# Kernel tuning notes

Measured on AMD Instinct MI355X. Metric: run time of the kernel, lower is better.

The kernel has to match this reference:

```python
import jax, jax.numpy as jnp
import numpy as np

ALPHA = 0.2        # LeakyReLU slope
N_NODES = 50000
N_REL = 500


def l2norm(x):
    n = jnp.linalg.norm(x, axis=1, keepdims=True)
    return x / jnp.maximum(n, 1e-12)


def gat_layer(x, edge, eemb, a, a2, concat):
    # x: [N, F]; edge: [2, E] (edge[0]=target, edge[1]=source); eemb: [E, R]
    dst = edge[0]
    h = jnp.concatenate([x[dst], x[edge[1]], eemb], axis=1)          # [E, 2F+R]
    m = h @ a.T                                                       # [E, out]
    p = -jax.nn.leaky_relu(m @ a2[0], ALPHA)                          # [E]
    e = jnp.exp(p)
    rowsum = jax.ops.segment_sum(e, dst, num_segments=N_NODES)       # [N]
    rowsum = jnp.where(rowsum == 0.0, 1e-12, rowsum)
    hp = jax.ops.segment_sum(e[:, None] * m, dst, num_segments=N_NODES) / rowsum[:, None]
    return jax.nn.elu(hp) if concat else hp


def setup_inputs() -> dict:
    key = jax.random.key(0)
    ks = jax.random.split(key, 12)
    E, ENH = 150000, 30000
    D, NHID, H = 200, 100, 2
    return {
        "entity_embeddings": jax.random.normal(ks[0], (N_NODES, D), jnp.float32),
        "relation_embeddings": jax.random.normal(ks[1], (N_REL, D), jnp.float32),
        "W_entities": jax.random.normal(ks[2], (D, NHID * H), jnp.float32) * 0.1,
        "W_gat": jax.random.normal(ks[3], (D, NHID * H), jnp.float32) * 0.1,
        "a_heads": jax.random.normal(ks[4], (H, NHID, 2 * D + D), jnp.float32) * 0.1,
        "a2_heads": jax.random.normal(ks[5], (H, 1, NHID), jnp.float32) * 0.1,
        "a_out": jax.random.normal(ks[6], (NHID * H, 3 * NHID * H), jnp.float32) * 0.1,
        "a2_out": jax.random.normal(ks[7], (1, NHID * H), jnp.float32) * 0.1,
        "batch_entities": jax.random.randint(ks[8], (20000,), 0, N_NODES),
        "edge_list": jax.random.randint(ks[9], (2, E), 0, N_NODES),
        "edge_type": jax.random.randint(ks[10], (E,), 0, N_REL),
        "train_indices_nhop": jax.random.randint(ks[11], (ENH, 4), 0, N_REL),
    }


def reference(entity_embeddings, relation_embeddings, W_entities, W_gat,
              a_heads, a2_heads, a_out, a2_out,
              batch_entities, edge_list, edge_type, train_indices_nhop):
    x = l2norm(entity_embeddings)
    # n-hop edges: (target, source) = (col 3, col 0); relation pair = (col 1, col 2)
    edge_nhop = jnp.stack([train_indices_nhop[:, 3], train_indices_nhop[:, 0]])
    edge_all = jnp.concatenate([edge_list, edge_nhop], axis=1)       # [2, E+Enh]
    eemb1 = jnp.concatenate([
        relation_embeddings[edge_type],
        relation_embeddings[train_indices_nhop[:, 1]] + relation_embeddings[train_indices_nhop[:, 2]],
    ], axis=0)
    # multi-head sparse attention (concat=True -> elu inside)
    heads = jax.vmap(lambda a, a2: gat_layer(x, edge_all, eemb1, a, a2, True))(a_heads, a2_heads)
    x1 = jnp.transpose(heads, (1, 0, 2)).reshape(x.shape[0], -1)     # [N, H*nhid]
    out_rel = relation_embeddings @ W_gat                             # [R, H*nhid]
    eemb2 = jnp.concatenate([
        out_rel[edge_type],
        out_rel[train_indices_nhop[:, 1]] + out_rel[train_indices_nhop[:, 2]],
    ], axis=0)
    out_ent = jax.nn.elu(gat_layer(x1, edge_all, eemb2, a_out, a2_out, False))
    mask = jnp.zeros((x.shape[0],), x.dtype).at[batch_entities].set(1.0)
    out_ent = l2norm(x @ W_entities + mask[:, None] * out_ent)
    return out_ent, out_rel, mask
```

## Files before the change

kernel.cpp:

```cpp
#include <hip/hip_runtime.h>
#include <hip/hip_bf16.h>
#include <math.h>

#define DD   200
#define NHID 100
#define OD   200
#define KP   224
#define PBS  224
#define LDSW 40

typedef __attribute__((ext_vector_type(8))) short short8;
typedef __attribute__((ext_vector_type(4))) float f32x4;

static inline int cdiv(int a, int b) { return (a + b - 1) / b; }

__device__ inline float toF(float x) { return x; }
__device__ inline float toF(__hip_bfloat16 x) { return __bfloat162float(x); }
__device__ inline void storeC(float v, float* p) { *p = v; }
__device__ inline void storeC(float v, __hip_bfloat16* p) { *p = __float2bfloat16(v); }
__device__ inline short bf16s(float f) {
    __hip_bfloat16 h = __float2bfloat16(f);
    short s; __builtin_memcpy(&s, &h, 2); return s;
}
__device__ inline float bfLo(unsigned u) { return __uint_as_float(u << 16); }
__device__ inline float bfHi(unsigned u) { return __uint_as_float(u & 0xFFFF0000u); }
__device__ inline float readlaneF(float v, int l) {
    return __uint_as_float((unsigned)__builtin_amdgcn_readlane((int)__float_as_uint(v), l));
}

__global__ __launch_bounds__(256)
void rownorm_inv_k(const float* __restrict__ in, float* __restrict__ sc, int M, int Dd)
{
    int wave = (blockIdx.x * blockDim.x + threadIdx.x) >> 6;
    int lane = threadIdx.x & 63;
    if (wave >= M) return;
    float ss = 0.f;
    for (int k = lane; k < Dd; k += 64) {
        float x = in[(size_t)wave * Dd + k];
        ss += x * x;
    }
    for (int o = 32; o > 0; o >>= 1) ss += __shfl_down(ss, o);
    if (lane == 0) sc[wave] = 1.f / fmaxf(sqrtf(ss), 1e-12f);
}

__global__ void prep_bt_l1(const float* __restrict__ ah, __hip_bfloat16* __restrict__ Bt)
{
    int c = blockIdx.x, k = threadIdx.x;
    if (k >= KP) return;
    int seg = c / 100, idx = c - seg * 100;
    int h = seg & 1, off = (seg >> 1) * 200;
    float v = (k < 200) ? ah[(size_t)(h * 100 + idx) * 600 + off + k] : 0.f;
    Bt[(size_t)c * KP + k] = __float2bfloat16(v);
}
__global__ void prep_bt_l2(const float* __restrict__ ao, __hip_bfloat16* __restrict__ Bt)
{
    int c = blockIdx.x, k = threadIdx.x;
    if (k >= KP) return;
    int row = (c < 200) ? c : c - 200;
    int off = (c < 200) ? 0 : 200;
    float v = (k < 200) ? ao[(size_t)row * 600 + off + k] : 0.f;
    Bt[(size_t)c * KP + k] = __float2bfloat16(v);
}
__global__ void prep_bt_fin(const float* __restrict__ W, __hip_bfloat16* __restrict__ Bt)
{
    int c = blockIdx.x, k = threadIdx.x;
    if (k >= KP) return;
    float v = (c < 200 && k < 200) ? W[(size_t)k * 200 + c] : 0.f;
    Bt[(size_t)c * KP + k] = __float2bfloat16(v);
}

__global__ __launch_bounds__(256)
void l1_both_k(const float* __restrict__ ent, const float* __restrict__ nscale,
               const __hip_bfloat16* __restrict__ Bt,
               const float* __restrict__ a2h,
               __hip_bfloat16* __restrict__ x1,
               __hip_bfloat16* __restrict__ pB,
               float* __restrict__ s1,
               int M)
{
    __shared__ __align__(16) __hip_bfloat16 Bs[400 * LDSW];
    int tid = threadIdx.x, wave = tid >> 6, lane = tid & 63;
    int quad = lane >> 4, l16 = lane & 15;
    int m0 = blockIdx.x * 64;
    int arow = m0 + wave * 16 + l16;
    bool rok = arow < M;
    float nsc = rok ? nscale[arow] : 0.f;
    const float* arp = ent + (size_t)arow * DD;

    f32x4 acc[25];
#pragma unroll
    for (int t = 0; t < 25; t++) acc[t] = (f32x4){0.f, 0.f, 0.f, 0.f};

    short8 stg[7];
#pragma unroll
    for (int i = 0; i < 7; i++) {
        int idx = tid + i * 256;
        if (idx < 1600) {
            int r = idx >> 2, c8 = idx & 3;
            stg[i] = *(const short8*)(Bt + (size_t)r * KP + c8 * 8);
        }
    }

    for (int ch = 0; ch < 7; ch++) {
#pragma unroll
        for (int i = 0; i < 7; i++) {
            int idx = tid + i * 256;
            if (idx < 1600) {
                int r = idx >> 2, c8 = idx & 3;
                *(short8*)(Bs + r * LDSW + c8 * 8) = stg[i];
            }
        }
        __syncthreads();
        if (ch < 6) {
            int kb2 = (ch + 1) * 32;
#pragma unroll
            for (int i = 0; i < 7; i++) {
                int idx = tid + i * 256;
                if (idx < 1600) {
                    int r = idx >> 2, c8 = idx & 3;
                    stg[i] = *(const short8*)(Bt + (size_t)r * KP + kb2 + c8 * 8);
                }
            }
        }
        int kb = ch * 32 + quad * 8;
        float av[8];
        if (rok && kb + 8 <= DD) {
            const float4* p = (const float4*)(arp + kb);
            float4 u0 = p[0], u1 = p[1];
            av[0] = u0.x; av[1] = u0.y; av[2] = u0.z; av[3] = u0.w;
            av[4] = u1.x; av[5] = u1.y; av[6] = u1.z; av[7] = u1.w;
        } else {
#pragma unroll
            for (int j = 0; j < 8; j++) av[j] = (rok && kb + j < DD) ? arp[kb + j] : 0.f;
        }
        short8 a;
#pragma unroll
        for (int j = 0; j < 8; j++) a[j] = bf16s(av[j] * nsc);
        const __hip_bfloat16* bp = Bs + (size_t)l16 * LDSW + quad * 8;
#pragma unroll
        for (int t = 0; t < 25; t++) {
            short8 b = *(const short8*)(bp + (size_t)t * 16 * LDSW);
            acc[t] = __builtin_amdgcn_mfma_f32_16x16x32_bf16(a, b, acc[t], 0, 0, 0);
        }
        __syncthreads();
    }

    int orow = m0 + wave * 16 + quad * 4;
    float d0[4] = {0,0,0,0}, d1[4] = {0,0,0,0}, d2[4] = {0,0,0,0}, d3[4] = {0,0,0,0};
#pragma unroll
    for (int t = 0; t < 25; t++) {
        int c = t * 16 + l16;
        int seg = c / 100, idx = c - seg * 100;
        float w = a2h[(seg & 1) * 100 + idx];
#pragma unroll
        for (int i = 0; i < 4; i++) {
            float v = acc[t][i];
            float vw = v * w;
            if (seg == 0) d0[i] += vw;
            else if (seg == 1) d1[i] += vw;
            else if (seg == 2) d2[i] += vw;
            else d3[i] += vw;
            int gm = orow + i;
            if (gm < M) {
                if (seg < 2) x1[(size_t)gm * KP + c] = __float2bfloat16(v);
                else pB[(size_t)gm * PBS + idx * 2 + (seg - 2)] = __float2bfloat16(v);
            }
        }
    }
#pragma unroll
    for (int msk = 1; msk < 16; msk <<= 1)
#pragma unroll
        for (int i = 0; i < 4; i++) {
            d0[i] += __shfl_xor(d0[i], msk);
            d1[i] += __shfl_xor(d1[i], msk);
            d2[i] += __shfl_xor(d2[i], msk);
            d3[i] += __shfl_xor(d3[i], msk);
        }
    if (l16 == 0)
#pragma unroll
        for (int i = 0; i < 4; i++) {
            int gm = orow + i;
            if (gm < M) {
                s1[gm] = d0[i]; s1[M + gm] = d1[i];
                float2 sv; sv.x = d2[i]; sv.y = d3[i];
                *(float2*)((char*)pB + (size_t)gm * (PBS * 2) + 400) = sv;
            }
        }
}

__global__ __launch_bounds__(256)
void l2_proj_k(const __hip_bfloat16* __restrict__ x1,
               const __hip_bfloat16* __restrict__ Bt,
               const float* __restrict__ a2o,
               float* __restrict__ x1A1,
               __hip_bfloat16* __restrict__ x1A2,
               float* __restrict__ s1, int M)
{
    __shared__ __align__(16) __hip_bfloat16 Bs[400 * LDSW];
    int tid = threadIdx.x, wave = tid >> 6, lane = tid & 63;
    int quad = lane >> 4, l16 = lane & 15;
    int m0 = blockIdx.x * 64;
    int arow = m0 + wave * 16 + l16;
    bool rok = arow < M;
    const __hip_bfloat16* arp = x1 + (size_t)arow * KP;

    f32x4 acc[25];
#pragma unroll
    for (int t = 0; t < 25; t++) acc[t] = (f32x4){0.f, 0.f, 0.f, 0.f};

    short8 stg[7];
#pragma unroll
    for (int i = 0; i < 7; i++) {
        int idx = tid + i * 256;
        if (idx < 1600) {
            int r = idx >> 2, c8 = idx & 3;
            stg[i] = *(const short8*)(Bt + (size_t)r * KP + c8 * 8);
        }
    }

    for (int ch = 0; ch < 7; ch++) {
#pragma unroll
        for (int i = 0; i < 7; i++) {
            int idx = tid + i * 256;
            if (idx < 1600) {
                int r = idx >> 2, c8 = idx & 3;
                *(short8*)(Bs + r * LDSW + c8 * 8) = stg[i];
            }
        }
        __syncthreads();
        if (ch < 6) {
            int kb2 = (ch + 1) * 32;
#pragma unroll
            for (int i = 0; i < 7; i++) {
                int idx = tid + i * 256;
                if (idx < 1600) {
                    int r = idx >> 2, c8 = idx & 3;
                    stg[i] = *(const short8*)(Bt + (size_t)r * KP + kb2 + c8 * 8);
                }
            }
        }
        int kb = ch * 32 + quad * 8;
        short8 a = (short8){0,0,0,0,0,0,0,0};
        if (rok) a = *(const short8*)(arp + kb);
        const __hip_bfloat16* bp = Bs + (size_t)l16 * LDSW + quad * 8;
#pragma unroll
        for (int t = 0; t < 25; t++) {
            short8 b = *(const short8*)(bp + (size_t)t * 16 * LDSW);
            acc[t] = __builtin_amdgcn_mfma_f32_16x16x32_bf16(a, b, acc[t], 0, 0, 0);
        }
        __syncthreads();
    }

    int orow = m0 + wave * 16 + quad * 4;
    float dA[4] = {0,0,0,0}, dB[4] = {0,0,0,0};
#pragma unroll
    for (int t = 0; t < 25; t++) {
        int c = t * 16 + l16;
        bool first = c < 200;
        int cc = first ? c : c - 200;
        float w = a2o[cc];
#pragma unroll
        for (int i = 0; i < 4; i++) {
            float v = acc[t][i];
            int gm = orow + i;
            if (first) {
                dA[i] += v * w;
                if (gm < M) x1A1[(size_t)gm * OD + c] = v;
            } else {
                dB[i] += v * w;
                if (gm < M) x1A2[(size_t)gm * PBS + cc] = __float2bfloat16(v);
            }
        }
    }
#pragma unroll
    for (int msk = 1; msk < 16; msk <<= 1)
#pragma unroll
        for (int i = 0; i < 4; i++) {
            dA[i] += __shfl_xor(dA[i], msk);
            dB[i] += __shfl_xor(dB[i], msk);
        }
    if (l16 == 0)
#pragma unroll
        for (int i = 0; i < 4; i++) {
            int gm = orow + i;
            if (gm < M) {
                s1[gm] = dA[i];
                *(float*)((char*)x1A2 + (size_t)gm * (PBS * 2) + 400) = dB[i];
            }
        }
}

__global__ __launch_bounds__(256)
void final_mfma_k(const float* __restrict__ ent, const float* __restrict__ nscale,
                  const __hip_bfloat16* __restrict__ Bt,
                  float* __restrict__ outent, int M)
{
    __shared__ __align__(16) __hip_bfloat16 Bs[208 * LDSW];
    int tid = threadIdx.x, wave = tid >> 6, lane = tid & 63;
    int quad = lane >> 4, l16 = lane & 15;
    int m0 = blockIdx.x * 64;
    int arow = m0 + wave * 16 + l16;
    bool rok = arow < M;
    float nsc = rok ? nscale[arow] : 0.f;
    const float* arp = ent + (size_t)arow * DD;

    f32x4 acc[13];
#pragma unroll
    for (int t = 0; t < 13; t++) acc[t] = (f32x4){0.f, 0.f, 0.f, 0.f};

    short8 stg[4];
#pragma unroll
    for (int i = 0; i < 4; i++) {
        int idx = tid + i * 256;
        if (idx < 832) {
            int r = idx >> 2, c8 = idx & 3;
            stg[i] = *(const short8*)(Bt + (size_t)r * KP + c8 * 8);
        }
    }

    for (int ch = 0; ch < 7; ch++) {
#pragma unroll
        for (int i = 0; i < 4; i++) {
            int idx = tid + i * 256;
            if (idx < 832) {
                int r = idx >> 2, c8 = idx & 3;
                *(short8*)(Bs + r * LDSW + c8 * 8) = stg[i];
            }
        }
        __syncthreads();
        if (ch < 6) {
            int kb2 = (ch + 1) * 32;
#pragma unroll
            for (int i = 0; i < 4; i++) {
                int idx = tid + i * 256;
                if (idx < 832) {
                    int r = idx >> 2, c8 = idx & 3;
                    stg[i] = *(const short8*)(Bt + (size_t)r * KP + kb2 + c8 * 8);
                }
            }
        }
        int kb = ch * 32 + quad * 8;
        float av[8];
        if (rok && kb + 8 <= DD) {
            const float4* p = (const float4*)(arp + kb);
            float4 u0 = p[0], u1 = p[1];
            av[0] = u0.x; av[1] = u0.y; av[2] = u0.z; av[3] = u0.w;
            av[4] = u1.x; av[5] = u1.y; av[6] = u1.z; av[7] = u1.w;
        } else {
#pragma unroll
            for (int j = 0; j < 8; j++) av[j] = (rok && kb + j < DD) ? arp[kb + j] : 0.f;
        }
        short8 a;
#pragma unroll
        for (int j = 0; j < 8; j++) a[j] = bf16s(av[j] * nsc);
        const __hip_bfloat16* bp = Bs + (size_t)l16 * LDSW + quad * 8;
#pragma unroll
        for (int t = 0; t < 13; t++) {
            short8 b = *(const short8*)(bp + (size_t)t * 16 * LDSW);
            acc[t] = __builtin_amdgcn_mfma_f32_16x16x32_bf16(a, b, acc[t], 0, 0, 0);
        }
        __syncthreads();
    }

    int orow = m0 + wave * 16 + quad * 4;
    float ss[4] = {0.f, 0.f, 0.f, 0.f};
#pragma unroll
    for (int t = 0; t < 13; t++) {
        int gn = t * 16 + l16;
#pragma unroll
        for (int i = 0; i < 4; i++) {
            int gm = orow + i;
            float v = 0.f;
            if (gn < OD && gm < M) v = acc[t][i] + outent[(size_t)gm * OD + gn];
            acc[t][i] = v;
            ss[i] += v * v;
        }
    }
#pragma unroll
    for (int msk = 1; msk < 16; msk <<= 1)
#pragma unroll
        for (int i = 0; i < 4; i++) ss[i] += __shfl_xor(ss[i], msk);
    float scl[4];
#pragma unroll
    for (int i = 0; i < 4; i++) scl[i] = 1.f / fmaxf(sqrtf(ss[i]), 1e-12f);
#pragma unroll
    for (int t = 0; t < 13; t++) {
        int gn = t * 16 + l16;
        if (gn >= OD) continue;
#pragma unroll
        for (int i = 0; i < 4; i++) {
            int gm = orow + i;
            if (gm < M) outent[(size_t)gm * OD + gn] = acc[t][i] * scl[i];
        }
    }
}

#define KPAD 48
template<bool BTr, typename AT, typename CT>
__global__ __launch_bounds__(256)
void gemm_mfma_k(const AT* __restrict__ A, int lda, const float* __restrict__ ascale,
                 const float* __restrict__ B, int ldb, int colOff,
                 CT* __restrict__ C, int ldc, int cs, int co,
                 int M, int Nc, int K)
{
    __shared__ __align__(16) __hip_bfloat16 As[64][KPAD];
    __shared__ __align__(16) __hip_bfloat16 Bs[64][KPAD];
    int tid  = threadIdx.x;
    int wave = tid >> 6, lane = tid & 63;
    int quad = lane >> 4, l16 = lane & 15;
    int n0 = blockIdx.x * 64, m0 = blockIdx.y * 64;
    f32x4 acc[4];
#pragma unroll
    for (int t = 0; t < 4; t++) acc[t] = (f32x4){0.f, 0.f, 0.f, 0.f};

    for (int k0 = 0; k0 < K; k0 += 32) {
        {
            int m = tid >> 2, kc = (tid & 3) * 8;
            int gm = m0 + m;
            float scale = (ascale && gm < M) ? ascale[gm] : 1.f;
#pragma unroll
            for (int j = 0; j < 8; j++) {
                int gk = k0 + kc + j;
                float v = 0.f;
                if (gm < M && gk < K) v = toF(A[(size_t)gm * lda + gk]) * scale;
                As[m][kc + j] = __float2bfloat16(v);
            }
        }
        if (BTr) {
            int n = tid >> 2, kc = (tid & 3) * 8;
            int gn = n0 + n;
#pragma unroll
            for (int j = 0; j < 8; j++) {
                int gk = k0 + kc + j;
                float v = 0.f;
                if (gn < Nc && gk < K) v = B[(size_t)gn * ldb + colOff + gk];
                Bs[n][kc + j] = __float2bfloat16(v);
            }
        } else {
            int n = tid & 63, kq = tid >> 6;
            int gn = n0 + n;
#pragma unroll
            for (int j = 0; j < 8; j++) {
                int gk = k0 + kq * 8 + j;
                float v = 0.f;
                if (gn < Nc && gk < K) v = B[(size_t)gk * ldb + gn];
                Bs[n][kq * 8 + j] = __float2bfloat16(v);
            }
        }
        __syncthreads();
        short8 a = *(const short8*)&As[wave * 16 + l16][quad * 8];
#pragma unroll
        for (int t = 0; t < 4; t++) {
            short8 b = *(const short8*)&Bs[t * 16 + l16][quad * 8];
            acc[t] = __builtin_amdgcn_mfma_f32_16x16x32_bf16(a, b, acc[t], 0, 0, 0);
        }
        __syncthreads();
    }
#pragma unroll
    for (int t = 0; t < 4; t++) {
        int gn = n0 + t * 16 + l16;
        if (gn >= Nc) continue;
#pragma unroll
        for (int i = 0; i < 4; i++) {
            int gm = m0 + wave * 16 + quad * 4 + i;
            if (gm < M) storeC(acc[t][i], &C[(size_t)gm * ldc + (size_t)gn * cs + co]);
        }
    }
}

template<typename T>
__global__ __launch_bounds__(256)
void rowdot_k(const T* __restrict__ mat, int ld, int coff, int ks,
              const float* __restrict__ vec,
              float* __restrict__ outp, int os, int oo, int M, int Dd)
{
    int wave = (blockIdx.x * blockDim.x + threadIdx.x) >> 6;
    int lane = threadIdx.x & 63;
    if (wave >= M) return;
    float s = 0.f;
    for (int k = lane; k < Dd; k += 64)
        s += toF(mat[(size_t)wave * ld + coff + (size_t)k * ks]) * vec[k];
    for (int o = 32; o > 0; o >>= 1) s += __shfl_down(s, o);
    if (lane == 0) outp[wave * os + oo] = s;
}

__device__ inline void decode_edge(const int* __restrict__ el, int E,
                                   const int* __restrict__ etype,
                                   const int* __restrict__ tin, int e,
                                   int& dst, int& src, int& r1, int& r2)
{
    if (e < E) { dst = el[e]; src = el[E + e]; r1 = etype[e]; r2 = -1; }
    else {
        int j = e - E;
        dst = tin[j * 4 + 3]; src = tin[j * 4 + 0];
        r1 = tin[j * 4 + 1];  r2 = tin[j * 4 + 2];
    }
}

__global__ void hist_k(const int* __restrict__ el, int E, const int* __restrict__ etype,
                       const int* __restrict__ tin, int Etot, int* __restrict__ cnt)
{
    int e = blockIdx.x * blockDim.x + threadIdx.x;
    if (e >= Etot) return;
    int dst, src, r1, r2; decode_edge(el, E, etype, tin, e, dst, src, r1, r2);
    atomicAdd(&cnt[dst], 1);
}

__global__ __launch_bounds__(1024)
void scan1_k(const int* __restrict__ cnt, int* __restrict__ start,
             int* __restrict__ aux, int n)
{
    __shared__ int tmp[1024];
    int i = blockIdx.x * 1024 + threadIdx.x;
    int v = (i < n) ? cnt[i] : 0;
    tmp[threadIdx.x] = v;
    __syncthreads();
    for (int o = 1; o < 1024; o <<= 1) {
        int t = (threadIdx.x >= (unsigned)o) ? tmp[threadIdx.x - o] : 0;
        __syncthreads();
        tmp[threadIdx.x] += t;
        __syncthreads();
    }
    if (i < n) start[i] = tmp[threadIdx.x] - v;
    if (threadIdx.x == 1023) aux[blockIdx.x] = tmp[1023];
}

__global__ void scan2_k(int* __restrict__ aux, int nb)
{
    if (threadIdx.x == 0 && blockIdx.x == 0) {
        int s = 0;
        for (int i = 0; i < nb; i++) { int v = aux[i]; aux[i] = s; s += v; }
    }
}

__global__ __launch_bounds__(1024)
void scan3_k(int* __restrict__ start, const int* __restrict__ aux, int n, int Etot)
{
    int i = blockIdx.x * 1024 + threadIdx.x;
    if (i < n) start[i] += aux[blockIdx.x];
    if (i == 0) start[n] = Etot;
}

__global__ void fill_k(const int* __restrict__ el, int E, const int* __restrict__ etype,
                       const int* __restrict__ tin, int Etot,
                       const int* __restrict__ start, int* __restrict__ fill,
                       int2* __restrict__ csr)
{
    int e = blockIdx.x * blockDim.x + threadIdx.x;
    if (e >= Etot) return;
    int dst, src, r1, r2; decode_edge(el, E, etype, tin, e, dst, src, r1, r2);
    int p = start[dst] + atomicAdd(&fill[dst], 1);
    unsigned r2s = (r2 >= 0) ? (unsigned)r2 : 0xFFFFu;
    csr[p] = make_int2(src, (int)((r2s << 16) | (unsigned)r1));
}

__global__ __launch_bounds__(256)
void gather_l1_k(const int* __restrict__ start, const int2* __restrict__ csr,
                 const float* __restrict__ s1,
                 const float* __restrict__ srel2,
                 const __hip_bfloat16* __restrict__ pB,
                 const float* __restrict__ rpf2,
                 __hip_bfloat16* __restrict__ x1, int N)
{
    int n = (blockIdx.x * blockDim.x + threadIdx.x) >> 6;
    int lane = threadIdx.x & 63;
    if (n >= N) return;
    int b0 = __builtin_amdgcn_readfirstlane(start[n]);
    int b1 = __builtin_amdgcn_readfirstlane(start[n + 1]);
    float s1h0 = s1[n], s1h1 = s1[N + n];
    float rsl0 = 0.f, rsl1 = 0.f;
    float2 acc0 = {0.f, 0.f};
    float2 acc1 = {0.f, 0.f};
    int k0 = lane;
    bool k1ok = lane < 36;
    int k1c = k1ok ? (lane + 64) : 0;

    for (int c0 = b0; c0 < b1; c0 += 64) {
        int cnt = min(64, b1 - c0);
        float w0 = 0.f, w1 = 0.f;
        int srcL = 0, eyL = 0;
        if (lane < cnt) {
            int2 eg = csr[c0 + lane];
            srcL = eg.x; eyL = eg.y;
            int r1 = eyL & 0xFFFF;
            unsigned r2u = (unsigned)eyL >> 16;
            float2 sA = *(const float2*)((const char*)pB + (size_t)(unsigned)srcL * (PBS * 2) + 400);
            float2 sr = *(const float2*)(srel2 + r1 * 2);
            float z0 = s1h0 + sA.x + sr.x;
            float z1 = s1h1 + sA.y + sr.y;
            if (r2u != 0xFFFFu) {
                float2 sr2v = *(const float2*)(srel2 + r2u * 2);
                z0 += sr2v.x; z1 += sr2v.y;
            }
            w0 = expf(-(z0 > 0.f ? z0 : 0.2f * z0));
            w1 = expf(-(z1 > 0.f ? z1 : 0.2f * z1));
            rsl0 += w0; rsl1 += w1;
        }
        for (int e0 = 0; e0 < cnt; e0 += 4) {
            int ec = min(4, cnt - e0);
            unsigned pw0[4], pw1[4];
#pragma unroll
            for (int u = 0; u < 4; u++) {
                if (u < ec) {
                    int s = __builtin_amdgcn_readlane(srcL, e0 + u);
                    const __hip_bfloat16* rA = pB + (size_t)(unsigned)s * PBS;
                    pw0[u] = *(const unsigned*)(rA + 2 * k0);
                    pw1[u] = *(const unsigned*)(rA + 2 * k1c);
                }
            }
#pragma unroll
            for (int u = 0; u < 4; u++) {
                if (u < ec) {
                    int ey = __builtin_amdgcn_readlane(eyL, e0 + u);
                    int r1 = ey & 0xFFFF;
                    unsigned r2u = (unsigned)ey >> 16;
                    float we0 = readlaneF(w0, e0 + u);
                    float we1 = readlaneF(w1, e0 + u);
                    const float2* q1 = (const float2*)(rpf2 + (unsigned)r1 * 200);
                    float2 q1a = q1[k0], q1b = q1[k1c];
                    float v00 = bfLo(pw0[u]) + q1a.x;
                    float v01 = bfHi(pw0[u]) + q1a.y;
                    float v10 = bfLo(pw1[u]) + q1b.x;
                    float v11 = bfHi(pw1[u]) + q1b.y;
                    if (r2u != 0xFFFFu) {
                        const float2* q2 = (const float2*)(rpf2 + r2u * 200);
                        float2 q2a = q2[k0], q2b = q2[k1c];
                        v00 += q2a.x; v01 += q2a.y;
                        v10 += q2b.x; v11 += q2b.y;
                    }
                    acc0.x += we0 * v00; acc0.y += we1 * v01;
                    acc1.x += we0 * v10; acc1.y += we1 * v11;
                }
            }
        }
    }

#pragma unroll
    for (int o = 1; o < 64; o <<= 1) {
        rsl0 += __shfl_xor(rsl0, o);
        rsl1 += __shfl_xor(rsl1, o);
    }
    float i0 = rsl0 > 0.f ? 1.f / rsl0 : 0.f;
    float i1 = rsl1 > 0.f ? 1.f / rsl1 : 0.f;
    __hip_bfloat16* xr = x1 + (size_t)n * KP;
    float hp;
    hp = rsl0 > 0.f ? toF(xr[k0]) + acc0.x * i0 : 0.f;
    xr[k0] = __float2bfloat16(hp > 0.f ? hp : expf(hp) - 1.f);
    hp = rsl1 > 0.f ? toF(xr[100 + k0]) + acc0.y * i1 : 0.f;
    xr[100 + k0] = __float2bfloat16(hp > 0.f ? hp : expf(hp) - 1.f);
    if (k1ok) {
        int k1 = lane + 64;
        hp = rsl0 > 0.f ? toF(xr[k1]) + acc1.x * i0 : 0.f;
        xr[k1] = __float2bfloat16(hp > 0.f ? hp : expf(hp) - 1.f);
        hp = rsl1 > 0.f ? toF(xr[100 + k1]) + acc1.y * i1 : 0.f;
        xr[100 + k1] = __float2bfloat16(hp > 0.f ? hp : expf(hp) - 1.f);
    }
}

__global__ __launch_bounds__(256)
void gather_l2_k(const int* __restrict__ start, const int2* __restrict__ csr,
                 const float* __restrict__ s1,
                 const float* __restrict__ srel,
                 const __hip_bfloat16* __restrict__ x1A2,
                 const float* __restrict__ rpf,
                 const float* __restrict__ maskf,
                 float* __restrict__ outent, int N)
{
    int n = (blockIdx.x * blockDim.x + threadIdx.x) >> 6;
    int lane = threadIdx.x & 63;
    if (n >= N) return;
    int b0 = __builtin_amdgcn_readfirstlane(start[n]);
    int b1 = __builtin_amdgcn_readfirstlane(start[n + 1]);
    float s1n = s1[n];
    float rsl = 0.f;
    float2 a0 = {0.f, 0.f};
    float2 a1 = {0.f, 0.f};
    int j0 = 2 * lane;
    bool j1ok = lane < 36;
    int j1 = j1ok ? (128 + 2 * lane) : 0;

    for (int c0 = b0; c0 < b1; c0 += 64) {
        int cnt = min(64, b1 - c0);
        float w = 0.f;
        int srcL = 0, eyL = 0;
        if (lane < cnt) {
            int2 eg = csr[c0 + lane];
            srcL = eg.x; eyL = eg.y;
            int r1 = eyL & 0xFFFF;
            unsigned r2u = (unsigned)eyL >> 16;
            float s2v = *(const float*)((const char*)x1A2 + (size_t)(unsigned)srcL * (PBS * 2) + 400);
            float sr = srel[r1];
            if (r2u != 0xFFFFu) sr += srel[r2u];
            float z = s1n + s2v + sr;
            w = expf(-(z > 0.f ? z : 0.2f * z));
            rsl += w;
        }
        for (int e0 = 0; e0 < cnt; e0 += 4) {
            int ec = min(4, cnt - e0);
            unsigned xw0[4], xw1[4];
#pragma unroll
            for (int u = 0; u < 4; u++) {
                if (u < ec) {
                    int s = __builtin_amdgcn_readlane(srcL, e0 + u);
                    const __hip_bfloat16* xs = x1A2 + (size_t)(unsigned)s * PBS;
                    xw0[u] = *(const unsigned*)(xs + j0);
                    xw1[u] = *(const unsigned*)(xs + j1);
                }
            }
#pragma unroll
            for (int u = 0; u < 4; u++) {
                if (u < ec) {
                    int ey = __builtin_amdgcn_readlane(eyL, e0 + u);
                    int r1 = ey & 0xFFFF;
                    unsigned r2u = (unsigned)ey >> 16;
                    float we = readlaneF(w, e0 + u);
                    const float* q1 = rpf + (unsigned)r1 * 200;
                    float2 q1a = *(const float2*)(q1 + j0);
                    float2 q1b = *(const float2*)(q1 + j1);
                    float v0x = bfLo(xw0[u]) + q1a.x;
                    float v0y = bfHi(xw0[u]) + q1a.y;
                    float v1x = bfLo(xw1[u]) + q1b.x;
                    float v1y = bfHi(xw1[u]) + q1b.y;
                    if (r2u != 0xFFFFu) {
                        const float* q2 = rpf + r2u * 200;
                        float2 q2a = *(const float2*)(q2 + j0);
                        float2 q2b = *(const float2*)(q2 + j1);
                        v0x += q2a.x; v0y += q2a.y;
                        v1x += q2b.x; v1y += q2b.y;
                    }
                    a0.x += we * v0x; a0.y += we * v0y;
                    a1.x += we * v1x; a1.y += we * v1y;
                }
            }
        }
    }

#pragma unroll
    for (int o = 1; o < 64; o <<= 1) rsl += __shfl_xor(rsl, o);
    float inv = rsl > 0.f ? 1.f / rsl : 0.f;
    float mk = maskf[n];
    float* orow = outent + (size_t)n * 200;
    {
        float2 o = *(const float2*)(orow + j0);
        float hpx = rsl > 0.f ? o.x + a0.x * inv : 0.f;
        float hpy = rsl > 0.f ? o.y + a0.y * inv : 0.f;
        float2 r;
        r.x = mk * (hpx > 0.f ? hpx : expf(hpx) - 1.f);
        r.y = mk * (hpy > 0.f ? hpy : expf(hpy) - 1.f);
        *(float2*)(orow + j0) = r;
    }
    if (j1ok) {
        float2 o = *(const float2*)(orow + j1);
        float hpx = rsl > 0.f ? o.x + a1.x * inv : 0.f;
        float hpy = rsl > 0.f ? o.y + a1.y * inv : 0.f;
        float2 r;
        r.x = mk * (hpx > 0.f ? hpx : expf(hpx) - 1.f);
        r.y = mk * (hpy > 0.f ? hpy : expf(hpy) - 1.f);
        *(float2*)(orow + j1) = r;
    }
}

__global__ void scatter_mask_k(const int* __restrict__ batch, int NB,
                               float* __restrict__ masko)
{
    int i = blockIdx.x * blockDim.x + threadIdx.x;
    if (i >= NB) return;
    masko[batch[i]] = 1.0f;
}

extern "C" void kernel_launch(void* const* d_in, const int* in_sizes, int n_in,
                              void* d_out, int out_size, void* d_ws, size_t ws_size,
                              hipStream_t stream)
{
    const float* ent      = (const float*)d_in[0];
    const float* rel      = (const float*)d_in[1];
    const float* W_ent    = (const float*)d_in[2];
    const float* W_gat    = (const float*)d_in[3];
    const float* a_heads  = (const float*)d_in[4];
    const float* a2_heads = (const float*)d_in[5];
    const float* a_out    = (const float*)d_in[6];
    const float* a2_out   = (const float*)d_in[7];
    const int* batch = (const int*)d_in[8];
    const int* el    = (const int*)d_in[9];
    const int* etype = (const int*)d_in[10];
    const int* tin   = (const int*)d_in[11];

    const int N   = in_sizes[0] / DD;
    const int R   = in_sizes[1] / DD;
    const int NB  = in_sizes[8];
    const int E   = in_sizes[9] / 2;
    const int ENH = in_sizes[11] / 4;
    const int Etot = E + ENH;

    char* ws = (char*)d_ws;
    size_t off = 0;
    auto take = [&](size_t bytes) { size_t o = off; off += (bytes + 255) & ~(size_t)255; return o; };
    size_t o_R1   = take((size_t)N * KP * 2);
    size_t o_R2   = take((size_t)N * PBS * 2);
    size_t o_rpf  = take((size_t)2 * R * 100 * 4);
    size_t o_bt1  = take((size_t)400 * KP * 2);
    size_t o_bt2  = take((size_t)400 * KP * 2);
    size_t o_btf  = take((size_t)208 * KP * 2);
    size_t o_nsc  = take((size_t)N * 4);
    size_t o_s1   = take((size_t)2 * N * 4);
    size_t o_srel = take((size_t)2 * R * 4);
    size_t o_csr  = take((size_t)Etot * 8);
    size_t o_str  = take((size_t)(N + 1) * 4);
    size_t o_aux  = take((size_t)64 * 4);

    __hip_bfloat16* x1   = (__hip_bfloat16*)(ws + o_R1);
    __hip_bfloat16* pB   = (__hip_bfloat16*)(ws + o_R2);
    __hip_bfloat16* x1A2 = (__hip_bfloat16*)(ws + o_R2);
    float* rpf2   = (float*)(ws + o_rpf);
    __hip_bfloat16* bt1 = (__hip_bfloat16*)(ws + o_bt1);
    __hip_bfloat16* bt2 = (__hip_bfloat16*)(ws + o_bt2);
    __hip_bfloat16* btf = (__hip_bfloat16*)(ws + o_btf);
    float* nscale = (float*)(ws + o_nsc);
    float* s1     = (float*)(ws + o_s1);
    float* srel2  = (float*)(ws + o_srel);
    int2*  csr    = (int2*)(ws + o_csr);
    int*   cnt    = (int*)(ws + o_s1);
    int*   startA = (int*)(ws + o_str);
    int*   aux    = (int*)(ws + o_aux);

    float* out       = (float*)d_out;
    float* out_ent   = out;
    float* out_rel_o = out + (size_t)N * OD;
    float* out_mask  = out + (size_t)N * OD + (size_t)R * OD;

    const int nblk = cdiv(N, 64);
    const int nbScan = cdiv(N, 1024);

    rownorm_inv_k<<<cdiv(N, 4), 256, 0, stream>>>(ent, nscale, N, DD);
    prep_bt_l1<<<400, 256, 0, stream>>>(a_heads, bt1);
    prep_bt_l2<<<400, 256, 0, stream>>>(a_out, bt2);
    prep_bt_fin<<<208, 256, 0, stream>>>(W_ent, btf);
    hipMemsetAsync(x1, 0, (size_t)N * KP * 2, stream);
    gemm_mfma_k<false, float, float><<<dim3(cdiv(OD, 64), cdiv(R, 64)), 256, 0, stream>>>(
        rel, DD, nullptr, W_gat, OD, 0, out_rel_o, OD, 1, 0, R, OD, DD);

    hipMemsetAsync(cnt, 0, (size_t)N * 4, stream);
    hist_k<<<cdiv(Etot, 256), 256, 0, stream>>>(el, E, etype, tin, Etot, cnt);
    scan1_k<<<nbScan, 1024, 0, stream>>>(cnt, startA, aux, N);
    scan2_k<<<1, 64, 0, stream>>>(aux, nbScan);
    scan3_k<<<nbScan, 1024, 0, stream>>>(startA, aux, N, Etot);
    hipMemsetAsync(cnt, 0, (size_t)N * 4, stream);
    fill_k<<<cdiv(Etot, 256), 256, 0, stream>>>(el, E, etype, tin, Etot, startA, cnt, csr);

    l1_both_k<<<nblk, 256, 0, stream>>>(ent, nscale, bt1, a2_heads, x1, pB, s1, N);
    for (int h = 0; h < 2; h++) {
        const float* ah  = a_heads + (size_t)h * NHID * 600;
        const float* a2h = a2_heads + (size_t)h * NHID;
        gemm_mfma_k<true, float, float><<<dim3(cdiv(NHID, 64), cdiv(R, 64)), 256, 0, stream>>>(
            rel, DD, nullptr, ah, 600, 400, rpf2, 200, 2, h, R, NHID, DD);
        rowdot_k<float><<<cdiv(R, 4), 256, 0, stream>>>(
            rpf2, 200, h, 2, a2h, srel2, 2, h, R, NHID);
    }
    gather_l1_k<<<cdiv(N, 4), 256, 0, stream>>>(
        startA, csr, s1, srel2, pB, rpf2, x1, N);

    l2_proj_k<<<nblk, 256, 0, stream>>>(x1, bt2, a2_out, out_ent, x1A2, s1, N);
    gemm_mfma_k<true, float, float><<<dim3(cdiv(OD, 64), cdiv(R, 64)), 256, 0, stream>>>(
        out_rel_o, OD, nullptr, a_out, 600, 400, rpf2, OD, 1, 0, R, OD, OD);
    rowdot_k<float><<<cdiv(R, 4), 256, 0, stream>>>(rpf2, OD, 0, 1, a2_out, srel2, 1, 0, R, OD);

    hipMemsetAsync(out_mask, 0, (size_t)N * 4, stream);
    scatter_mask_k<<<cdiv(NB, 256), 256, 0, stream>>>(batch, NB, out_mask);
    gather_l2_k<<<cdiv(N, 4), 256, 0, stream>>>(
        startA, csr, s1, srel2, x1A2, rpf2, out_mask, out_ent, N);

    final_mfma_k<<<nblk, 256, 0, stream>>>(ent, nscale, btf, out_ent, N);
}
```

Before: 515.3 us.

## Fuse final entity projection into layer-1 GEMM and normalize in gather_l2

```diff
diff --git a/kernel.cpp b/kernel.cpp
--- a/kernel.cpp
+++ b/kernel.cpp
@@ -6,7 +6,7 @@
 #define NHID 100
 #define OD   200
 #define KP   224
-#define PBS  224
+#define PBS  448
 #define LDSW 40
 
 typedef __attribute__((ext_vector_type(8))) short short8;
@@ -78,7 +78,7 @@
                float* __restrict__ s1,
                int M)
 {
-    __shared__ __align__(16) __hip_bfloat16 Bs[400 * LDSW];
+    __shared__ __align__(16) __hip_bfloat16 Bs[608 * LDSW];
     int tid = threadIdx.x, wave = tid >> 6, lane = tid & 63;
     int quad = lane >> 4, l16 = lane & 15;
     int m0 = blockIdx.x * 64;
@@ -87,41 +87,9 @@
     float nsc = rok ? nscale[arow] : 0.f;
     const float* arp = ent + (size_t)arow * DD;
 
-    f32x4 acc[25];
-#pragma unroll
-    for (int t = 0; t < 25; t++) acc[t] = (f32x4){0.f, 0.f, 0.f, 0.f};
-
-    short8 stg[7];
-#pragma unroll
-    for (int i = 0; i < 7; i++) {
-        int idx = tid + i * 256;
-        if (idx < 1600) {
-            int r = idx >> 2, c8 = idx & 3;
-            stg[i] = *(const short8*)(Bt + (size_t)r * KP + c8 * 8);
-        }
-    }
-
+    short8 abuf[7];
+#pragma unroll
     for (int ch = 0; ch < 7; ch++) {
-#pragma unroll
-        for (int i = 0; i < 7; i++) {
-            int idx = tid + i * 256;
-            if (idx < 1600) {
-                int r = idx >> 2, c8 = idx & 3;
-                *(short8*)(Bs + r * LDSW + c8 * 8) = stg[i];
-            }
-        }
-        __syncthreads();
-        if (ch < 6) {
-            int kb2 = (ch + 1) * 32;
-#pragma unroll
-            for (int i = 0; i < 7; i++) {
-                int idx = tid + i * 256;
-                if (idx < 1600) {
-                    int r = idx >> 2, c8 = idx & 3;
-                    stg[i] = *(const short8*)(Bt + (size_t)r * KP + kb2 + c8 * 8);
-                }
-            }
-        }
         int kb = ch * 32 + quad * 8;
         float av[8];
         if (rok && kb + 8 <= DD) {
@@ -136,13 +104,40 @@
         short8 a;
 #pragma unroll
         for (int j = 0; j < 8; j++) a[j] = bf16s(av[j] * nsc);
+        abuf[ch] = a;
+    }
+
+    f32x4 acc[38];
+#pragma unroll
+    for (int t = 0; t < 38; t++) acc[t] = (f32x4){0.f, 0.f, 0.f, 0.f};
+
+    for (int ch = 0; ch < 7; ch++) {
+        short8 stg[10];
+#pragma unroll
+        for (int i = 0; i < 10; i++) {
+            int idx = tid + i * 256;
+            if (idx < 2432) {
+                int r = idx >> 2, c8 = idx & 3;
+                stg[i] = *(const short8*)(Bt + (size_t)r * KP + ch * 32 + c8 * 8);
+            }
+        }
+        __syncthreads();
+#pragma unroll
+        for (int i = 0; i < 10; i++) {
+            int idx = tid + i * 256;
+            if (idx < 2432) {
+                int r = idx >> 2, c8 = idx & 3;
+                *(short8*)(Bs + r * LDSW + c8 * 8) = stg[i];
+            }
+        }
+        __syncthreads();
         const __hip_bfloat16* bp = Bs + (size_t)l16 * LDSW + quad * 8;
-#pragma unroll
-        for (int t = 0; t < 25; t++) {
+        short8 a = abuf[ch];
+#pragma unroll
+        for (int t = 0; t < 38; t++) {
             short8 b = *(const short8*)(bp + (size_t)t * 16 * LDSW);
             acc[t] = __builtin_amdgcn_mfma_f32_16x16x32_bf16(a, b, acc[t], 0, 0, 0);
         }
-        __syncthreads();
     }
 
     int orow = m0 + wave * 16 + quad * 4;
@@ -168,6 +163,16 @@
         }
     }
 #pragma unroll
+    for (int t = 25; t < 38; t++) {
+        int c2 = (t - 25) * 16 + l16;
+#pragma unroll
+        for (int i = 0; i < 4; i++) {
+            int gm = orow + i;
+            if (c2 < OD && gm < M)
+                pB[(size_t)gm * PBS + 224 + c2] = __float2bfloat16(acc[t][i]);
+        }
+    }
+#pragma unroll
     for (int msk = 1; msk < 16; msk <<= 1)
 #pragma unroll
         for (int i = 0; i < 4; i++) {
@@ -204,21 +209,29 @@
     bool rok = arow < M;
     const __hip_bfloat16* arp = x1 + (size_t)arow * KP;
 
+    short8 abuf[7];
+#pragma unroll
+    for (int ch = 0; ch < 7; ch++) {
+        short8 a = (short8){0,0,0,0,0,0,0,0};
+        if (rok) a = *(const short8*)(arp + ch * 32 + quad * 8);
+        abuf[ch] = a;
+    }
+
     f32x4 acc[25];
 #pragma unroll
     for (int t = 0; t < 25; t++) acc[t] = (f32x4){0.f, 0.f, 0.f, 0.f};
 
-    short8 stg[7];
-#pragma unroll
-    for (int i = 0; i < 7; i++) {
-        int idx = tid + i * 256;
-        if (idx < 1600) {
-            int r = idx >> 2, c8 = idx & 3;
-            stg[i] = *(const short8*)(Bt + (size_t)r * KP + c8 * 8);
-        }
-    }
-
     for (int ch = 0; ch < 7; ch++) {
+        short8 stg[7];
+#pragma unroll
+        for (int i = 0; i < 7; i++) {
+            int idx = tid + i * 256;
+            if (idx < 1600) {
+                int r = idx >> 2, c8 = idx & 3;
+                stg[i] = *(const short8*)(Bt + (size_t)r * KP + ch * 32 + c8 * 8);
+            }
+        }
+        __syncthreads();
 #pragma unroll
         for (int i = 0; i < 7; i++) {
             int idx = tid + i * 256;
@@ -228,27 +241,13 @@
             }
         }
         __syncthreads();
-        if (ch < 6) {
-            int kb2 = (ch + 1) * 32;
-#pragma unroll
-            for (int i = 0; i < 7; i++) {
-                int idx = tid + i * 256;
-                if (idx < 1600) {
-                    int r = idx >> 2, c8 = idx & 3;
-                    stg[i] = *(const short8*)(Bt + (size_t)r * KP + kb2 + c8 * 8);
-                }
-            }
-        }
-        int kb = ch * 32 + quad * 8;
-        short8 a = (short8){0,0,0,0,0,0,0,0};
-        if (rok) a = *(const short8*)(arp + kb);
         const __hip_bfloat16* bp = Bs + (size_t)l16 * LDSW + quad * 8;
+        short8 a = abuf[ch];
 #pragma unroll
         for (int t = 0; t < 25; t++) {
             short8 b = *(const short8*)(bp + (size_t)t * 16 * LDSW);
             acc[t] = __builtin_amdgcn_mfma_f32_16x16x32_bf16(a, b, acc[t], 0, 0, 0);
         }
-        __syncthreads();
     }
 
     int orow = m0 + wave * 16 + quad * 4;
@@ -288,111 +287,6 @@
                 *(float*)((char*)x1A2 + (size_t)gm * (PBS * 2) + 400) = dB[i];
             }
         }
-}
-
-__global__ __launch_bounds__(256)
-void final_mfma_k(const float* __restrict__ ent, const float* __restrict__ nscale,
-                  const __hip_bfloat16* __restrict__ Bt,
-                  float* __restrict__ outent, int M)
-{
-    __shared__ __align__(16) __hip_bfloat16 Bs[208 * LDSW];
-    int tid = threadIdx.x, wave = tid >> 6, lane = tid & 63;
-    int quad = lane >> 4, l16 = lane & 15;
-    int m0 = blockIdx.x * 64;
-    int arow = m0 + wave * 16 + l16;
-    bool rok = arow < M;
-    float nsc = rok ? nscale[arow] : 0.f;
-    const float* arp = ent + (size_t)arow * DD;
-
-    f32x4 acc[13];
-#pragma unroll
-    for (int t = 0; t < 13; t++) acc[t] = (f32x4){0.f, 0.f, 0.f, 0.f};
-
-    short8 stg[4];
-#pragma unroll
-    for (int i = 0; i < 4; i++) {
-        int idx = tid + i * 256;
-        if (idx < 832) {
-            int r = idx >> 2, c8 = idx & 3;
-            stg[i] = *(const short8*)(Bt + (size_t)r * KP + c8 * 8);
-        }
-    }
-
-    for (int ch = 0; ch < 7; ch++) {
-#pragma unroll
-        for (int i = 0; i < 4; i++) {
-            int idx = tid + i * 256;
-            if (idx < 832) {
-                int r = idx >> 2, c8 = idx & 3;
-                *(short8*)(Bs + r * LDSW + c8 * 8) = stg[i];
-            }
-        }
-        __syncthreads();
-        if (ch < 6) {
-            int kb2 = (ch + 1) * 32;
-#pragma unroll
-            for (int i = 0; i < 4; i++) {
-                int idx = tid + i * 256;
-                if (idx < 832) {
-                    int r = idx >> 2, c8 = idx & 3;
-                    stg[i] = *(const short8*)(Bt + (size_t)r * KP + kb2 + c8 * 8);
-                }
-            }
-        }
-        int kb = ch * 32 + quad * 8;
-        float av[8];
-        if (rok && kb + 8 <= DD) {
-            const float4* p = (const float4*)(arp + kb);
-            float4 u0 = p[0], u1 = p[1];
-            av[0] = u0.x; av[1] = u0.y; av[2] = u0.z; av[3] = u0.w;
-            av[4] = u1.x; av[5] = u1.y; av[6] = u1.z; av[7] = u1.w;
-        } else {
-#pragma unroll
-            for (int j = 0; j < 8; j++) av[j] = (rok && kb + j < DD) ? arp[kb + j] : 0.f;
-        }
-        short8 a;
-#pragma unroll
-        for (int j = 0; j < 8; j++) a[j] = bf16s(av[j] * nsc);
-        const __hip_bfloat16* bp = Bs + (size_t)l16 * LDSW + quad * 8;
-#pragma unroll
-        for (int t = 0; t < 13; t++) {
-            short8 b = *(const short8*)(bp + (size_t)t * 16 * LDSW);
-            acc[t] = __builtin_amdgcn_mfma_f32_16x16x32_bf16(a, b, acc[t], 0, 0, 0);
-        }
-        __syncthreads();
-    }
-
-    int orow = m0 + wave * 16 + quad * 4;
-    float ss[4] = {0.f, 0.f, 0.f, 0.f};
-#pragma unroll
-    for (int t = 0; t < 13; t++) {
-        int gn = t * 16 + l16;
-#pragma unroll
-        for (int i = 0; i < 4; i++) {
-            int gm = orow + i;
-            float v = 0.f;
-            if (gn < OD && gm < M) v = acc[t][i] + outent[(size_t)gm * OD + gn];
-            acc[t][i] = v;
-            ss[i] += v * v;
-        }
-    }
-#pragma unroll
-    for (int msk = 1; msk < 16; msk <<= 1)
-#pragma unroll
-        for (int i = 0; i < 4; i++) ss[i] += __shfl_xor(ss[i], msk);
-    float scl[4];
-#pragma unroll
-    for (int i = 0; i < 4; i++) scl[i] = 1.f / fmaxf(sqrtf(ss[i]), 1e-12f);
-#pragma unroll
-    for (int t = 0; t < 13; t++) {
-        int gn = t * 16 + l16;
-        if (gn >= OD) continue;
-#pragma unroll
-        for (int i = 0; i < 4; i++) {
-            int gm = orow + i;
-            if (gm < M) outent[(size_t)gm * OD + gn] = acc[t][i] * scl[i];
-        }
-    }
 }
 
 #define KPAD 48
@@ -740,23 +634,33 @@
     float inv = rsl > 0.f ? 1.f / rsl : 0.f;
     float mk = maskf[n];
     float* orow = outent + (size_t)n * 200;
-    {
-        float2 o = *(const float2*)(orow + j0);
-        float hpx = rsl > 0.f ? o.x + a0.x * inv : 0.f;
-        float hpy = rsl > 0.f ? o.y + a0.y * inv : 0.f;
-        float2 r;
-        r.x = mk * (hpx > 0.f ? hpx : expf(hpx) - 1.f);
-        r.y = mk * (hpy > 0.f ? hpy : expf(hpy) - 1.f);
-        *(float2*)(orow + j0) = r;
-    }
+    const __hip_bfloat16* ew = x1A2 + (size_t)n * PBS + 224;
+
+    float2 o0 = *(const float2*)(orow + j0);
+    unsigned e0b = *(const unsigned*)(ew + j0);
+    float h0x = rsl > 0.f ? o0.x + a0.x * inv : 0.f;
+    float h0y = rsl > 0.f ? o0.y + a0.y * inv : 0.f;
+    float v0x = mk * (h0x > 0.f ? h0x : expf(h0x) - 1.f) + bfLo(e0b);
+    float v0y = mk * (h0y > 0.f ? h0y : expf(h0y) - 1.f) + bfHi(e0b);
+    float ssq = v0x * v0x + v0y * v0y;
+    float v1x = 0.f, v1y = 0.f;
     if (j1ok) {
-        float2 o = *(const float2*)(orow + j1);
-        float hpx = rsl > 0.f ? o.x + a1.x * inv : 0.f;
-        float hpy = rsl > 0.f ? o.y + a1.y * inv : 0.f;
-        float2 r;
-        r.x = mk * (hpx > 0.f ? hpx : expf(hpx) - 1.f);
-        r.y = mk * (hpy > 0.f ? hpy : expf(hpy) - 1.f);
-        *(float2*)(orow + j1) = r;
+        float2 o1 = *(const float2*)(orow + j1);
+        unsigned e1b = *(const unsigned*)(ew + j1);
+        float h1x = rsl > 0.f ? o1.x + a1.x * inv : 0.f;
+        float h1y = rsl > 0.f ? o1.y + a1.y * inv : 0.f;
+        v1x = mk * (h1x > 0.f ? h1x : expf(h1x) - 1.f) + bfLo(e1b);
+        v1y = mk * (h1y > 0.f ? h1y : expf(h1y) - 1.f) + bfHi(e1b);
+        ssq += v1x * v1x + v1y * v1y;
+    }
+#pragma unroll
+    for (int o = 1; o < 64; o <<= 1) ssq += __shfl_xor(ssq, o);
+    float sc = 1.f / fmaxf(sqrtf(ssq), 1e-12f);
+    float2 r0; r0.x = v0x * sc; r0.y = v0y * sc;
+    *(float2*)(orow + j0) = r0;
+    if (j1ok) {
+        float2 r1; r1.x = v1x * sc; r1.y = v1y * sc;
+        *(float2*)(orow + j1) = r1;
     }
 }
 
@@ -799,8 +703,8 @@
     size_t o_R2   = take((size_t)N * PBS * 2);
     size_t o_rpf  = take((size_t)2 * R * 100 * 4);
     size_t o_bt1  = take((size_t)400 * KP * 2);
+    size_t o_btf  = take((size_t)208 * KP * 2);
     size_t o_bt2  = take((size_t)400 * KP * 2);
-    size_t o_btf  = take((size_t)208 * KP * 2);
     size_t o_nsc  = take((size_t)N * 4);
     size_t o_s1   = take((size_t)2 * N * 4);
     size_t o_srel = take((size_t)2 * R * 4);
@@ -813,8 +717,8 @@
     __hip_bfloat16* x1A2 = (__hip_bfloat16*)(ws + o_R2);
     float* rpf2   = (float*)(ws + o_rpf);
     __hip_bfloat16* bt1 = (__hip_bfloat16*)(ws + o_bt1);
+    __hip_bfloat16* btf = (__hip_bfloat16*)(ws + o_btf);
     __hip_bfloat16* bt2 = (__hip_bfloat16*)(ws + o_bt2);
-    __hip_bfloat16* btf = (__hip_bfloat16*)(ws + o_btf);
     float* nscale = (float*)(ws + o_nsc);
     float* s1     = (float*)(ws + o_s1);
     float* srel2  = (float*)(ws + o_srel);
@@ -833,8 +737,8 @@
 
     rownorm_inv_k<<<cdiv(N, 4), 256, 0, stream>>>(ent, nscale, N, DD);
     prep_bt_l1<<<400, 256, 0, stream>>>(a_heads, bt1);
+    prep_bt_fin<<<208, 256, 0, stream>>>(W_ent, btf);
     prep_bt_l2<<<400, 256, 0, stream>>>(a_out, bt2);
-    prep_bt_fin<<<208, 256, 0, stream>>>(W_ent, btf);
     hipMemsetAsync(x1, 0, (size_t)N * KP * 2, stream);
     gemm_mfma_k<false, float, float><<<dim3(cdiv(OD, 64), cdiv(R, 64)), 256, 0, stream>>>(
         rel, DD, nullptr, W_gat, OD, 0, out_rel_o, OD, 1, 0, R, OD, DD);
@@ -868,6 +772,4 @@
     scatter_mask_k<<<cdiv(NB, 256), 256, 0, stream>>>(batch, NB, out_mask);
     gather_l2_k<<<cdiv(N, 4), 256, 0, stream>>>(
         startA, csr, s1, srel2, x1A2, rpf2, out_mask, out_ent, N);
-
-    final_mfma_k<<<nblk, 256, 0, stream>>>(ent, nscale, btf, out_ent, N);
-}
+}
```

After: 580.5 us. 1.13x slower.
